# Kernel optimization log

Hardware: AMD Instinct MI355X
Metric: run time of the kernel (lower is better)

The kernel has to match this reference:

```python
import math
import jax, jax.numpy as jnp
import numpy as np
from jax import lax

B, T, D, S, N_SLOTS, N_ITERS = 16, 4096, 768, 768, 16, 8
THR, EPS = 0.5, 1e-8
SCALE = D ** -0.5
NEG = -jnp.finfo(jnp.float32).max


def ln(x, g, b):
    mu = x.mean(-1, keepdims=True)
    var = ((x - mu) ** 2).mean(-1, keepdims=True)
    return (x - mu) / jnp.sqrt(var + 1e-5) * g + b


def gru_cell(u, h, wih, whh, bih, bhh):
    # torch GRUCell: r,z,n gate ordering
    gi = u @ wih.T + bih
    gh = h @ whh.T + bhh
    ir, iz, inn = jnp.split(gi, 3, axis=-1)
    hr, hz, hn = jnp.split(gh, 3, axis=-1)
    r = jax.nn.sigmoid(ir + hr)
    z = jax.nn.sigmoid(iz + hz)
    n = jnp.tanh(inn + r * hn)
    return (1.0 - z) * n + z * h


def sa_step(slots, k, v, p, slot_mask, context_mask):
    q = ln(slots, p['lsg'], p['lsb']) @ p['Wq'].T
    dots = jnp.einsum('bid,bjd->bij', q, k) * SCALE  # [B, n_slots, T]
    dots = jnp.where(context_mask[:, None, :], dots, NEG)
    if slot_mask is not None:
        dots = jnp.where(slot_mask[:, :, None], dots, NEG)
    attn_vis = jax.nn.softmax(dots, axis=1)  # softmax over SLOTS (inverted attn)
    attn = attn_vis + EPS
    attn = attn / attn.sum(-1, keepdims=True)
    updates = jnp.einsum('bjd,bij->bid', v, attn)
    b, n, d = slots.shape
    h = gru_cell(updates.reshape(b * n, d), slots.reshape(b * n, d),
                 p['gwih'], p['gwhh'], p['gbih'], p['gbhh'])
    slots = h.reshape(b, n, d)
    pre = ln(slots, p['lfg'], p['lfb'])
    slots = slots + (jax.nn.relu(pre @ p['w1'].T + p['b1']) @ p['w2'].T + p['b2'])
    return slots, attn_vis


def cluster_single(slots, attn, slot_mask):
    sl = lax.stop_gradient(slots)  # torch no_grad block
    ns = sl / jnp.clip(jnp.linalg.norm(sl, axis=-1, keepdims=True), 1e-12)
    smm = (slot_mask[:, :, None] & slot_mask[:, None, :]).astype(jnp.float32)
    dist = 1.0 - jnp.einsum('bnd,bmd->bnm', ns, ns)
    dist = jnp.where(smm > 0, dist, 2.0)
    adj = (dist < THR).astype(jnp.float32) * smm
    for _ in range(math.ceil(math.log2(N_SLOTS))):  # transitive closure by squaring
        adj = jnp.minimum(adj @ adj, 1.0) * smm
    cum = jnp.cumsum(adj, axis=1)
    cm = adj * (cum <= 1.0)  # keep first row of each connected component
    counts = (cm > 0).any(axis=2).sum(axis=1)
    reset = counts < 3
    eye = jnp.eye(N_SLOTS, dtype=jnp.float32)[None] * slot_mask[:, :, None].astype(jnp.float32)
    cm = jnp.where(reset[:, None, None], eye, cm)
    cw = cm / jnp.clip(cm.sum(axis=2, keepdims=True), 1.0)
    cm = lax.stop_gradient(cm)
    cw = lax.stop_gradient(cw)
    means = cw @ slots          # grads flow through slots only
    cattn = cm @ attn           # grads flow through attn only
    out_mask = (cm > 0).any(axis=2) & slot_mask
    return means, cattn, out_mask


def setup_inputs() -> dict:
    key = jax.random.key(0)
    ks = jax.random.split(key, 16)
    sc = 0.02
    return {
        'x': jax.random.normal(ks[0], (B, T, D), jnp.float32),
        'context_mask': jnp.ones((B, T), jnp.bool_),
        'n_slots': N_SLOTS,
        'slots_init': jax.random.normal(ks[1], (N_SLOTS, S), jnp.float32),
        'Wk': jax.random.normal(ks[2], (S, D), jnp.float32) * sc,
        'Wv': jax.random.normal(ks[3], (S, D), jnp.float32) * sc,
        'Wq': jax.random.normal(ks[4], (S, S), jnp.float32) * sc,
        'gwih': jax.random.normal(ks[5], (3 * S, S), jnp.float32) * sc,
        'gwhh': jax.random.normal(ks[6], (3 * S, S), jnp.float32) * sc,
        'gbih': jnp.zeros((3 * S,), jnp.float32),
        'gbhh': jnp.zeros((3 * S,), jnp.float32),
        'w1': jax.random.normal(ks[7], (4 * S, S), jnp.float32) * sc,
        'b1': jnp.zeros((4 * S,), jnp.float32),
        'w2': jax.random.normal(ks[8], (S, 4 * S), jnp.float32) * sc,
        'b2': jnp.zeros((S,), jnp.float32),
        'lin_g': jnp.ones((D,), jnp.float32), 'lin_b': jnp.zeros((D,), jnp.float32),
        'lsg': jnp.ones((S,), jnp.float32), 'lsb': jnp.zeros((S,), jnp.float32),
        'lfg': jnp.ones((S,), jnp.float32), 'lfb': jnp.zeros((S,), jnp.float32),
    }


def reference(x, context_mask, n_slots, slots_init, Wk, Wv, Wq, gwih, gwhh,
              gbih, gbhh, w1, b1, w2, b2, lin_g, lin_b, lsg, lsb, lfg, lfb):
    p = dict(Wq=Wq, gwih=gwih, gwhh=gwhh, gbih=gbih, gbhh=gbhh,
             w1=w1, b1=b1, w2=w2, b2=b2, lsg=lsg, lsb=lsb, lfg=lfg, lfb=lfb)
    xn = ln(x, lin_g, lin_b)
    init_slots = jnp.broadcast_to(slots_init[None], (x.shape[0], N_SLOTS, S))
    k = xn @ Wk.T
    v = xn @ Wv.T
    slots = init_slots
    for _ in range(N_ITERS):
        slots, attn = sa_step(slots, k, v, p, None, context_mask)
    # implicit differentiation trick
    slots = lax.stop_gradient(slots) - lax.stop_gradient(init_slots) + init_slots
    slot_mask = jnp.ones((x.shape[0], N_SLOTS), jnp.bool_)
    slots, attn = sa_step(slots, k, v, p, slot_mask, context_mask)
    slots, attn, slot_mask = cluster_single(slots, attn, slot_mask)
    attn_map = jnp.transpose(attn, (0, 2, 1))  # [B, T, n_slots]
    return slots, attn_map, slot_mask
```

## Files before the change

### kernel.cpp

```cpp
#include <hip/hip_runtime.h>
#include <hip/hip_bf16.h>

typedef __hip_bfloat16 bf16;
typedef __attribute__((ext_vector_type(4))) float f32x4;
typedef __attribute__((ext_vector_type(8))) short s16x8;
typedef unsigned int u32;
typedef unsigned short u16;

#define B_ 16
#define T_ 4096
#define D_ 768
#define S_ 768
#define NS 16
#define NIT 9
#define NCHUNK 16
#define TCH 256
#define EPS 1e-8f
#define SCALE 0.036084391824351615f

__device__ __forceinline__ void gld16(const void* g, void* l) {
    __builtin_amdgcn_global_load_lds((const __attribute__((address_space(1))) u32*)g,
                                     (__attribute__((address_space(3))) u32*)l, 16, 0, 0);
}

__device__ __forceinline__ u16 bfbits(float x) {
    bf16 h = __float2bfloat16(x);
    return *reinterpret_cast<u16*>(&h);
}

__global__ void __launch_bounds__(256) cvt_all_kernel(
    const float* __restrict__ wq, const float* __restrict__ wk, const float* __restrict__ wv,
    const float* __restrict__ gwih, const float* __restrict__ gwhh,
    const float* __restrict__ w1, const float* __restrict__ w2,
    bf16* __restrict__ wq_b, bf16* __restrict__ wkv_b,
    bf16* __restrict__ gwih_b, bf16* __restrict__ gwhh_b,
    bf16* __restrict__ w1_b, bf16* __restrict__ w2_b)
{
    int i = blockIdx.x * 256 + threadIdx.x;
    const int NW = 589824, NG = 1769472, NM = 2359296;
    if (i < NW) { wq_b[i] = __float2bfloat16(wq[i]); return; }
    i -= NW;
    if (i < NW) { wkv_b[i] = __float2bfloat16(wk[i]); return; }
    i -= NW;
    if (i < NW) { wkv_b[NW + i] = __float2bfloat16(wv[i]); return; }
    i -= NW;
    if (i < NG) { gwih_b[i] = __float2bfloat16(gwih[i]); return; }
    i -= NG;
    if (i < NG) { gwhh_b[i] = __float2bfloat16(gwhh[i]); return; }
    i -= NG;
    if (i < NM) { w1_b[i] = __float2bfloat16(w1[i]); return; }
    i -= NM;
    w2_b[i] = __float2bfloat16(w2[i]);
}

__global__ void __launch_bounds__(256) ln768_kernel(
    const float* __restrict__ x, const float* __restrict__ g,
    const float* __restrict__ bta, bf16* __restrict__ out)
{
    int wid = threadIdx.x >> 6, lane = threadIdx.x & 63;
    int row = blockIdx.x * 4 + wid;
    const float4* xr = (const float4*)(x + (size_t)row * 768);
    float4 v[3];
    float s = 0.f;
    #pragma unroll
    for (int i = 0; i < 3; ++i) {
        v[i] = xr[lane + i * 64];
        s += v[i].x + v[i].y + v[i].z + v[i].w;
    }
    #pragma unroll
    for (int off = 1; off < 64; off <<= 1) s += __shfl_xor(s, off);
    float mu = s * (1.f / 768.f);
    float q = 0.f;
    #pragma unroll
    for (int i = 0; i < 3; ++i) {
        float a = v[i].x - mu, b = v[i].y - mu, c = v[i].z - mu, d = v[i].w - mu;
        q += a * a + b * b + c * c + d * d;
    }
    #pragma unroll
    for (int off = 1; off < 64; off <<= 1) q += __shfl_xor(q, off);
    float rs = rsqrtf(q * (1.f / 768.f) + 1e-5f);
    ushort4* orow = (ushort4*)(out + (size_t)row * 768);
    const float4* gg = (const float4*)g;
    const float4* bb = (const float4*)bta;
    #pragma unroll
    for (int i = 0; i < 3; ++i) {
        float4 gv = gg[lane + i * 64], bv = bb[lane + i * 64];
        ushort4 o;
        o.x = bfbits((v[i].x - mu) * rs * gv.x + bv.x);
        o.y = bfbits((v[i].y - mu) * rs * gv.y + bv.y);
        o.z = bfbits((v[i].z - mu) * rs * gv.z + bv.z);
        o.w = bfbits((v[i].w - mu) * rs * gv.w + bv.w);
        orow[lane + i * 64] = o;
    }
}

__global__ void __launch_bounds__(512) gemm256_kernel(
    const bf16* __restrict__ A, const bf16* __restrict__ W,
    bf16* __restrict__ kout, bf16* __restrict__ vTout, float* __restrict__ vsum)
{
    __shared__ char smem[49152];
    __shared__ float vs_l[128];
    bf16* As = (bf16*)smem;
    bf16* Bs = (bf16*)(smem + 32768);
    int tid = threadIdx.x, lane = tid & 63, wid = tid >> 6;
    int bid = blockIdx.x;
    int xcd = bid & 7, idx = bid >> 3;
    int mt = xcd * 32 + idx / 12;
    int nt = idx % 12;
    int bm0 = mt * 256, bn0 = nt * 128;
    int wr = wid >> 1, wc = wid & 1;
    int g = lane >> 4, r15 = lane & 15;
    const f32x4 vzero = {0.f, 0.f, 0.f, 0.f};
    f32x4 acc[4][4];
    #pragma unroll
    for (int m = 0; m < 4; ++m)
        #pragma unroll
        for (int n = 0; n < 4; ++n) acc[m][n] = vzero;

    for (int kt = 0; kt < 768; kt += 64) {
        __syncthreads();
        #pragma unroll
        for (int i = 0; i < 4; ++i) {
            int s0 = i * 512 + wid * 64;
            int o = (s0 + lane) * 16;
            int r = o >> 7, cb = o & 127;
            int cbs = cb ^ ((r & 7) << 4);
            gld16(A + (size_t)(bm0 + r) * 768 + kt + (cbs >> 1), (char*)As + (size_t)s0 * 16);
        }
        #pragma unroll
        for (int i = 0; i < 2; ++i) {
            int s0 = i * 512 + wid * 64;
            int o = (s0 + lane) * 16;
            int r = o >> 7, cb = o & 127;
            int cbs = cb ^ ((r & 7) << 4);
            gld16(W + (size_t)(bn0 + r) * 768 + kt + (cbs >> 1), (char*)Bs + (size_t)s0 * 16);
        }
        asm volatile("s_waitcnt vmcnt(0)" ::: "memory");
        __syncthreads();
        #pragma unroll
        for (int kk2 = 0; kk2 < 2; ++kk2) {
            s16x8 af[4], bfr[4];
            #pragma unroll
            for (int m = 0; m < 4; ++m) {
                int r = wr * 64 + m * 16 + r15;
                int p = r * 128 + ((kk2 * 64 + g * 16) ^ ((r & 7) << 4));
                af[m] = *(const s16x8*)((const char*)As + p);
            }
            #pragma unroll
            for (int n = 0; n < 4; ++n) {
                int r = wc * 64 + n * 16 + r15;
                int p = r * 128 + ((kk2 * 64 + g * 16) ^ ((r & 7) << 4));
                bfr[n] = *(const s16x8*)((const char*)Bs + p);
            }
            #pragma unroll
            for (int m = 0; m < 4; ++m)
                #pragma unroll
                for (int n = 0; n < 4; ++n)
                    acc[m][n] = __builtin_amdgcn_mfma_f32_16x16x32_bf16(af[m], bfr[n], acc[m][n], 0, 0, 0);
        }
    }

    bool is_v = (bn0 >= 768);
    float* Ct = (float*)smem;
    int bq = bm0 >> 12;
    int tloc = bm0 & 4095;
    if (is_v && tid < 128) vs_l[tid] = 0.f;
    #pragma unroll
    for (int q = 0; q < 4; ++q) {
        __syncthreads();
        if (wr == q) {
            #pragma unroll
            for (int m = 0; m < 4; ++m)
                #pragma unroll
                for (int n = 0; n < 4; ++n)
                    #pragma unroll
                    for (int j = 0; j < 4; ++j)
                        Ct[(m * 16 + g * 4 + j) * 132 + wc * 64 + n * 16 + r15] = acc[m][n][j];
        }
        __syncthreads();
        if (!is_v) {
            int r = tid >> 3, cq = tid & 7;
            u16 tmp[16];
            #pragma unroll
            for (int i = 0; i < 4; ++i) {
                f32x4 vv = *(const f32x4*)&Ct[r * 132 + cq * 16 + i * 4];
                #pragma unroll
                for (int jj = 0; jj < 4; ++jj) tmp[i * 4 + jj] = bfbits(vv[jj]);
            }
            s16x8 o0, o1;
            #pragma unroll
            for (int i = 0; i < 8; ++i) { o0[i] = (short)tmp[i]; o1[i] = (short)tmp[8 + i]; }
            bf16* dst = kout + (size_t)(bm0 + q * 64 + r) * 768 + bn0 + cq * 16;
            *(s16x8*)dst = o0;
            *(s16x8*)(dst + 8) = o1;
        } else {
            int d = tid >> 2, tq = tid & 3;
            float ssum = 0.f;
            u16 tmp[16];
            #pragma unroll
            for (int i = 0; i < 16; ++i) {
                float f = Ct[(tq * 16 + i) * 132 + d];
                ssum += f;
                tmp[i] = bfbits(f);
            }
            s16x8 o0, o1;
            #pragma unroll
            for (int i = 0; i < 8; ++i) { o0[i] = (short)tmp[i]; o1[i] = (short)tmp[8 + i]; }
            bf16* dst = vTout + ((size_t)bq * 768 + (bn0 - 768) + d) * (size_t)T_
                        + tloc + q * 64 + tq * 16;
            *(s16x8*)dst = o0;
            *(s16x8*)(dst + 8) = o1;
            atomicAdd(&vs_l[d], ssum);
        }
    }
    if (is_v) {
        __syncthreads();
        if (tid < 128) atomicAdd(vsum + bq * 768 + (bn0 - 768) + tid, vs_l[tid]);
    }
}

__global__ void init_slots_kernel(const float* __restrict__ si,
                                  float* __restrict__ slots, bf16* __restrict__ slots_bf)
{
    int idx = blockIdx.x * 256 + threadIdx.x;
    float v = si[idx % (NS * S_)];
    slots[idx] = v;
    slots_bf[idx] = __float2bfloat16(v);
}

__global__ void __launch_bounds__(256) ln_gemm_kernel(
    const float* __restrict__ xin, const float* __restrict__ gam, const float* __restrict__ bet,
    const bf16* __restrict__ W, const float* __restrict__ bias,
    bf16* __restrict__ out, int N, int relu)
{
    __shared__ bf16 As[16 * 768];
    __shared__ bf16 Ws[2][64 * 64];
    int tid = threadIdx.x;
    int bx = blockIdx.x, bn0 = blockIdx.y * 64;
    int row = tid >> 4, li = tid & 15;
    const float* xr = xin + (size_t)(bx * 16 + row) * 768;
    float vals[48];
    float s = 0.f;
    #pragma unroll
    for (int i = 0; i < 48; ++i) { vals[i] = xr[li + i * 16]; s += vals[i]; }
    #pragma unroll
    for (int m = 1; m < 16; m <<= 1) s += __shfl_xor(s, m);
    float mu = s * (1.f / 768.f);
    float q = 0.f;
    #pragma unroll
    for (int i = 0; i < 48; ++i) { float d = vals[i] - mu; q += d * d; }
    #pragma unroll
    for (int m = 1; m < 16; m <<= 1) q += __shfl_xor(q, m);
    float rs = rsqrtf(q * (1.f / 768.f) + 1e-5f);
    #pragma unroll
    for (int i = 0; i < 48; ++i) {
        int c = li + i * 16;
        float v = (vals[i] - mu) * rs * gam[c] + bet[c];
        *(u16*)((char*)As + row * 1536 + ((c * 2) ^ ((row & 7) << 4))) = bfbits(v);
    }
    int lane = tid & 63, wid = tid >> 6;
    int g = lane >> 4, s15 = lane & 15;
    auto stageW = [&](int kt, int buf) {
        #pragma unroll
        for (int i = 0; i < 2; ++i) {
            int s0 = i * 256 + wid * 64;
            int o = (s0 + lane) * 16;
            int r = o >> 7, cb = o & 127;
            int cbs = cb ^ ((r & 7) << 4);
            gld16(W + (size_t)(bn0 + r) * 768 + kt + (cbs >> 1),
                  (char*)Ws[buf] + (size_t)s0 * 16);
        }
    };
    stageW(0, 0);
    asm volatile("s_waitcnt vmcnt(0)" ::: "memory");
    __syncthreads();
    f32x4 acc = {0.f, 0.f, 0.f, 0.f};
    int rb = wid * 16 + s15;
    for (int t = 0; t < 12; ++t) {
        int cur = t & 1;
        if (t < 11) stageW((t + 1) * 64, cur ^ 1);
        #pragma unroll
        for (int kk2 = 0; kk2 < 2; ++kk2) {
            int kabs = t * 64 + kk2 * 32;
            s16x8 af = *(const s16x8*)((const char*)As + s15 * 1536 +
                                       ((kabs * 2 + g * 16) ^ ((s15 & 7) << 4)));
            s16x8 bf_ = *(const s16x8*)((const char*)Ws[cur] + rb * 128 +
                                        ((kk2 * 64 + g * 16) ^ ((rb & 7) << 4)));
            acc = __builtin_amdgcn_mfma_f32_16x16x32_bf16(af, bf_, acc, 0, 0, 0);
        }
        asm volatile("s_waitcnt vmcnt(0)" ::: "memory");
        __syncthreads();
    }
    int cn = bn0 + rb;
    float bv = bias ? bias[cn] : 0.f;
    #pragma unroll
    for (int j = 0; j < 4; ++j) {
        float val = acc[j] + bv;
        if (relu) val = fmaxf(val, 0.f);
        out[(size_t)(bx * 16 + g * 4 + j) * N + cn] = __float2bfloat16(val);
    }
}

__global__ void __launch_bounds__(256) gru_fused16_kernel(
    const bf16* __restrict__ upd, const bf16* __restrict__ slotsA_bf,
    const bf16* __restrict__ Wih, const bf16* __restrict__ Whh,
    const float* __restrict__ bih, const float* __restrict__ bhh,
    const float* __restrict__ slotsA, float* __restrict__ slotsB)
{
    __shared__ char sm[53248];
    int tid = threadIdx.x, lane = tid & 63, wid = tid >> 6;
    int g = lane >> 4, r15 = lane & 15;
    int bm0 = blockIdx.x * 16, bn0 = blockIdx.y * 64;
    const f32x4 vz = {0.f, 0.f, 0.f, 0.f};
    f32x4 acc[6] = {vz, vz, vz, vz, vz, vz};

    for (int kt = 0; kt < 768; kt += 64) {
        __syncthreads();
        #pragma unroll
        for (int i = 0; i < 13; ++i) {
            int s0 = i * 256 + wid * 64;
            int seg = s0 + lane;
            const bf16* src;
            if (seg < 256) {
                int ls = seg & 127;
                int o = ls * 16;
                int r = o >> 7, cb = o & 127;
                int cbs = cb ^ ((r & 7) << 4);
                const bf16* base = (seg < 128) ? upd : slotsA_bf;
                src = base + (size_t)(bm0 + r) * 768 + kt + (cbs >> 1);
            } else {
                int ws = seg - 256;
                int p = ws >> 9, qq = ws & 511;
                int o = qq * 16;
                int r = o >> 7, cb = o & 127;
                int cbs = cb ^ ((r & 7) << 4);
                src = (p < 3)
                    ? Wih + (size_t)(p * 768 + bn0 + r) * 768 + kt + (cbs >> 1)
                    : Whh + (size_t)((p - 3) * 768 + bn0 + r) * 768 + kt + (cbs >> 1);
            }
            gld16(src, sm + (size_t)s0 * 16);
        }
        asm volatile("s_waitcnt vmcnt(0)" ::: "memory");
        __syncthreads();
        #pragma unroll
        for (int kk2 = 0; kk2 < 2; ++kk2) {
            int pa = r15 * 128 + ((kk2 * 64 + g * 16) ^ ((r15 & 7) << 4));
            s16x8 au = *(const s16x8*)(sm + pa);
            s16x8 ah = *(const s16x8*)(sm + 2048 + pa);
            int rb = wid * 16 + r15;
            int pb = rb * 128 + ((kk2 * 64 + g * 16) ^ ((rb & 7) << 4));
            #pragma unroll
            for (int p = 0; p < 6; ++p) {
                s16x8 wf = *(const s16x8*)(sm + 4096 + p * 8192 + pb);
                acc[p] = __builtin_amdgcn_mfma_f32_16x16x32_bf16(
                    (p < 3) ? au : ah, wf, acc[p], 0, 0, 0);
            }
        }
    }
    int cn = bn0 + wid * 16 + r15;
    float bir = bih[cn], biz = bih[768 + cn], bin_ = bih[1536 + cn];
    float bhr = bhh[cn], bhz = bhh[768 + cn], bhn = bhh[1536 + cn];
    #pragma unroll
    for (int j = 0; j < 4; ++j) {
        int m = bm0 + g * 4 + j;
        float ir = acc[0][j] + bir, iz = acc[1][j] + biz, inn = acc[2][j] + bin_;
        float hr = acc[3][j] + bhr, hz = acc[4][j] + bhz, hn = acc[5][j] + bhn;
        float rg = 1.f / (1.f + expf(-(ir + hr)));
        float z  = 1.f / (1.f + expf(-(iz + hz)));
        float nn = tanhf(inn + rg * hn);
        float h  = slotsA[(size_t)m * 768 + cn];
        slotsB[(size_t)m * 768 + cn] = (1.f - z) * nn + z * h;
    }
}

__device__ __forceinline__ void skinny_body(
    const bf16* A, const bf16* Bm, const float* bias, const float* Cin,
    float* Cf, bf16* Cb, int N, int K, int bm0, int bn0, int relu,
    bf16* As, bf16* Bs)
{
    int tid = threadIdx.x, lane = tid & 63, wid = tid >> 6;
    int g = lane >> 4, r15 = lane & 15;
    f32x4 acc = {0.f, 0.f, 0.f, 0.f};
    for (int kt = 0; kt < K; kt += 64) {
        __syncthreads();
        #pragma unroll
        for (int i = 0; i < 3; ++i) {
            int s0 = i * 256 + wid * 64;
            if (s0 < 640) {
                int o = (s0 + lane) * 16;
                if (o < 2048) {
                    int r = o >> 7, cb = o & 127;
                    int cbs = cb ^ ((r & 7) << 4);
                    gld16(A + (size_t)(bm0 + r) * K + kt + (cbs >> 1), (char*)As + (size_t)s0 * 16);
                } else {
                    int ob = o - 2048;
                    int r = ob >> 7, cb = ob & 127;
                    int cbs = cb ^ ((r & 7) << 4);
                    gld16(Bm + (size_t)(bn0 + r) * K + kt + (cbs >> 1),
                          (char*)Bs + (size_t)(s0 * 16 - 2048));
                }
            }
        }
        asm volatile("s_waitcnt vmcnt(0)" ::: "memory");
        __syncthreads();
        #pragma unroll
        for (int kk = 0; kk < 64; kk += 32) {
            int pa = r15 * 128 + ((kk * 2 + g * 16) ^ ((r15 & 7) << 4));
            s16x8 af = *(const s16x8*)((const char*)As + pa);
            int rb = wid * 16 + r15;
            int pb = rb * 128 + ((kk * 2 + g * 16) ^ ((rb & 7) << 4));
            s16x8 bfr = *(const s16x8*)((const char*)Bs + pb);
            acc = __builtin_amdgcn_mfma_f32_16x16x32_bf16(af, bfr, acc, 0, 0, 0);
        }
    }
    int cn = bn0 + wid * 16 + r15;
    float bv = bias ? bias[cn] : 0.f;
    #pragma unroll
    for (int j = 0; j < 4; ++j) {
        int cm = bm0 + g * 4 + j;
        size_t ci = (size_t)cm * N + cn;
        float val = acc[j] + bv;
        if (Cin) val += Cin[ci];
        if (relu) val = fmaxf(val, 0.f);
        if (Cf) Cf[ci] = val;
        if (Cb) Cb[ci] = __float2bfloat16(val);
    }
}

__global__ void __launch_bounds__(256) mlp2_kernel(
    const bf16* __restrict__ h1, const bf16* __restrict__ W2, const float* __restrict__ b2,
    const float* __restrict__ slotsB, float* __restrict__ slotsA, bf16* __restrict__ slotsA_bf)
{
    __shared__ bf16 As[16 * 64];
    __shared__ bf16 Bs[64 * 64];
    skinny_body(h1, W2, b2, slotsB, slotsA, slotsA_bf, 768, 3072,
                blockIdx.x * 16, blockIdx.y * 64, 0, As, Bs);
}

__global__ void __launch_bounds__(256) fused_attn_kernel(
    const bf16* __restrict__ q_bf, const bf16* __restrict__ k_bf, const bf16* __restrict__ vT,
    float* __restrict__ pU, float* __restrict__ prs, float* __restrict__ avis, int write_avis)
{
    __shared__ char smem[131072];
    bf16* ks0 = (bf16*)smem;
    bf16* ks1 = (bf16*)(smem + 49152);
    bf16* qs  = (bf16*)(smem + 98304);
    char* aL  = smem + 122880;
    __shared__ float rsw[2][16];
    int tid = threadIdx.x, lane = tid & 63, wid = tid >> 6;
    int b = blockIdx.x >> 4, chunk = blockIdx.x & 15;
    int t0 = chunk * TCH;
    int g = lane >> 4, s15 = lane & 15;
    const bf16* qb  = q_bf + (size_t)b * 16 * 768;
    const bf16* kb  = k_bf + (size_t)b * T_ * 768;
    const bf16* vtb = vT + (size_t)b * 768 * (size_t)T_;

    auto stage_k = [&](int tb, bf16* dst) {
        #pragma unroll
        for (int i = 0; i < 12; ++i) {
            int s0 = i * 256 + wid * 64;
            int o = (s0 + lane) * 16;
            int r = o / 1536, cb = o % 1536;
            int cbs = cb ^ ((r & 7) << 4);
            gld16(kb + (size_t)(tb + r) * 768 + (cbs >> 1), (char*)dst + (size_t)s0 * 16);
        }
    };
    auto stage_v = [&](int tb, bf16* dst) {
        #pragma unroll
        for (int i = 0; i < 12; ++i) {
            int s0 = i * 256 + wid * 64;
            int o = (s0 + lane) * 16;
            int d = o >> 6, cb = o & 63;
            int cbs = cb ^ ((d & 3) << 4);
            gld16(vtb + (size_t)d * T_ + tb + (cbs >> 1), (char*)dst + (size_t)s0 * 16);
        }
    };

    #pragma unroll
    for (int i = 0; i < 6; ++i) {
        int s0 = i * 256 + wid * 64;
        int o = (s0 + lane) * 16;
        int r = o / 1536, cb = o % 1536;
        int cbs = cb ^ ((r & 7) << 4);
        gld16(qb + (size_t)r * 768 + (cbs >> 1), (char*)qs + (size_t)s0 * 16);
    }
    stage_k(t0, ks0);
    asm volatile("s_waitcnt vmcnt(0)" ::: "memory");
    __syncthreads();

    const f32x4 vzero = {0.f, 0.f, 0.f, 0.f};
    float rs_acc = 0.f;

    for (int ts = 0; ts < 8; ++ts) {
        bf16* cur = (ts & 1) ? ks1 : ks0;
        bf16* nxt = (ts & 1) ? ks0 : ks1;
        if (ts < 7) stage_k(t0 + (ts + 1) * 32, nxt);
        if (wid < 2) {
            f32x4 dacc = vzero;
            #pragma unroll
            for (int kk = 0; kk < 768; kk += 32) {
                int rk = wid * 16 + s15;
                int pk = rk * 1536 + ((kk * 2 + g * 16) ^ ((rk & 7) << 4));
                s16x8 kf = *(const s16x8*)((const char*)cur + pk);
                int pq = s15 * 1536 + ((kk * 2 + g * 16) ^ ((s15 & 7) << 4));
                s16x8 qf = *(const s16x8*)((const char*)qs + pq);
                dacc = __builtin_amdgcn_mfma_f32_16x16x32_bf16(kf, qf, dacc, 0, 0, 0);
            }
            float d0 = dacc[0] * SCALE, d1 = dacc[1] * SCALE,
                  d2 = dacc[2] * SCALE, d3 = dacc[3] * SCALE;
            float m0 = d0, m1 = d1, m2 = d2, m3 = d3;
            #pragma unroll
            for (int off = 1; off < 16; off <<= 1) {
                m0 = fmaxf(m0, __shfl_xor(m0, off));
                m1 = fmaxf(m1, __shfl_xor(m1, off));
                m2 = fmaxf(m2, __shfl_xor(m2, off));
                m3 = fmaxf(m3, __shfl_xor(m3, off));
            }
            float e0 = expf(d0 - m0), e1 = expf(d1 - m1), e2 = expf(d2 - m2), e3 = expf(d3 - m3);
            float q0 = e0, q1 = e1, q2 = e2, q3 = e3;
            #pragma unroll
            for (int off = 1; off < 16; off <<= 1) {
                q0 += __shfl_xor(q0, off);
                q1 += __shfl_xor(q1, off);
                q2 += __shfl_xor(q2, off);
                q3 += __shfl_xor(q3, off);
            }
            float a0 = e0 / q0, a1 = e1 / q1, a2 = e2 / q2, a3 = e3 / q3;
            rs_acc += a0 + a1 + a2 + a3;
            int tl = wid * 16 + g * 4;
            ushort2 p0, p1;
            p0.x = bfbits(a0); p0.y = bfbits(a1);
            p1.x = bfbits(a2); p1.y = bfbits(a3);
            int sw = (s15 & 3) << 4;
            char* aS = aL + ts * 1024;
            *(ushort2*)(aS + s15 * 64 + ((tl * 2) ^ sw))       = p0;
            *(ushort2*)(aS + s15 * 64 + (((tl + 2) * 2) ^ sw)) = p1;
            if (write_avis) {
                f32x4 wv = {a0, a1, a2, a3};
                *(f32x4*)(avis + (size_t)(b * 16 + s15) * T_ + t0 + ts * 32 + tl) = wv;
            }
        }
        asm volatile("s_waitcnt vmcnt(0)" ::: "memory");
        __syncthreads();
    }

    f32x4 uacc[12];
    #pragma unroll
    for (int i = 0; i < 12; ++i) uacc[i] = vzero;
    stage_v(t0, ks0);
    asm volatile("s_waitcnt vmcnt(0)" ::: "memory");
    __syncthreads();
    for (int ts = 0; ts < 8; ++ts) {
        bf16* cur = (ts & 1) ? ks1 : ks0;
        bf16* nxt = (ts & 1) ? ks0 : ks1;
        if (ts < 7) stage_v(t0 + (ts + 1) * 32, nxt);
        {
            int pa = ts * 1024 + s15 * 64 + ((g * 16) ^ ((s15 & 3) << 4));
            s16x8 afr = *(const s16x8*)(aL + pa);
            #pragma unroll
            for (int i = 0; i < 12; ++i) {
                int d = (wid * 12 + i) * 16 + s15;
                int pv = d * 64 + ((g * 16) ^ ((d & 3) << 4));
                s16x8 vf = *(const s16x8*)((const char*)cur + pv);
                uacc[i] = __builtin_amdgcn_mfma_f32_16x16x32_bf16(vf, afr, uacc[i], 0, 0, 0);
            }
        }
        asm volatile("s_waitcnt vmcnt(0)" ::: "memory");
        __syncthreads();
    }

    float* pUb = pU + (size_t)(b * 16 + chunk) * 768 * 16;
    #pragma unroll
    for (int i = 0; i < 12; ++i) {
        int dbase = (wid * 12 + i) * 16 + g * 4;
        #pragma unroll
        for (int j = 0; j < 4; ++j)
            pUb[(size_t)(dbase + j) * 16 + s15] = uacc[i][j];
    }
    rs_acc += __shfl_xor(rs_acc, 16);
    rs_acc += __shfl_xor(rs_acc, 32);
    if (wid < 2 && lane < 16) rsw[wid][s15] = rs_acc;
    __syncthreads();
    if (tid < 16) prs[(b * 16 + chunk) * 16 + tid] = rsw[0][tid] + rsw[1][tid];
}

__global__ void __launch_bounds__(256) attn_reduce_kernel(
    const float* __restrict__ pU, const float* __restrict__ prs,
    const float* __restrict__ vsum, bf16* __restrict__ upd)
{
    int idx = blockIdx.x * 256 + threadIdx.x;
    int d = idx % 768;
    int s = (idx / 768) & 15;
    int b = idx / (768 * 16);
    float su = 0.f;
    #pragma unroll
    for (int c = 0; c < 16; ++c) su += pU[((size_t)(b * 16 + c) * 768 + d) * 16 + s];
    float rs = 0.f;
    #pragma unroll
    for (int c = 0; c < 16; ++c) rs += prs[(b * 16 + c) * 16 + s];
    float val = (su + EPS * vsum[b * 768 + d]) / (rs + T_ * EPS);
    upd[idx] = __float2bfloat16(val);
}

__global__ void __launch_bounds__(256) cluster_kernel(
    const float* __restrict__ slots, float* __restrict__ out_slots,
    float* __restrict__ out_mask, float* __restrict__ cm_g)
{
    int b = blockIdx.x;
    __shared__ float s[16][768];
    __shared__ float inv[16];
    __shared__ float adj[16][16], tmp[16][16], cw[16][16];
    __shared__ int reset_s;
    const float* sb = slots + (size_t)b * 16 * 768;
    for (int i = threadIdx.x; i < 16 * 768; i += 256) s[i / 768][i % 768] = sb[i];
    __syncthreads();
    if (threadIdx.x < 16) {
        float q = 0.f;
        for (int d = 0; d < 768; ++d) q += s[threadIdx.x][d] * s[threadIdx.x][d];
        inv[threadIdx.x] = 1.f / fmaxf(sqrtf(q), 1e-12f);
    }
    __syncthreads();
    int n = threadIdx.x >> 4, m = threadIdx.x & 15;
    float dot = 0.f;
    for (int d = 0; d < 768; ++d) dot += s[n][d] * s[m][d];
    dot *= inv[n] * inv[m];
    adj[n][m] = ((1.f - dot) < 0.5f) ? 1.f : 0.f;
    __syncthreads();
    #pragma unroll
    for (int it = 0; it < 4; ++it) {
        float t = 0.f;
        #pragma unroll
        for (int j = 0; j < 16; ++j) t += adj[n][j] * adj[j][m];
        tmp[n][m] = fminf(t, 1.f);
        __syncthreads();
        adj[n][m] = tmp[n][m];
        __syncthreads();
    }
    if (threadIdx.x < 16) {
        int mm = threadIdx.x;
        float run = 0.f;
        for (int nn = 0; nn < 16; ++nn) {
            run += adj[nn][mm];
            tmp[nn][mm] = adj[nn][mm] * ((run <= 1.f) ? 1.f : 0.f);
        }
    }
    __syncthreads();
    if (threadIdx.x == 0) {
        int cnt2 = 0;
        for (int nn = 0; nn < 16; ++nn) {
            bool any = false;
            for (int j = 0; j < 16; ++j) any = any || (tmp[nn][j] > 0.f);
            cnt2 += any ? 1 : 0;
        }
        reset_s = (cnt2 < 3) ? 1 : 0;
    }
    __syncthreads();
    if (reset_s) tmp[n][m] = (n == m) ? 1.f : 0.f;
    __syncthreads();
    if (threadIdx.x < 16) {
        float rs = 0.f;
        for (int j = 0; j < 16; ++j) rs += tmp[threadIdx.x][j];
        rs = fmaxf(rs, 1.f);
        for (int j = 0; j < 16; ++j) cw[threadIdx.x][j] = tmp[threadIdx.x][j] / rs;
        bool any = false;
        for (int j = 0; j < 16; ++j) any = any || (tmp[threadIdx.x][j] > 0.f);
        out_mask[b * 16 + threadIdx.x] = any ? 1.f : 0.f;
    }
    cm_g[b * 256 + threadIdx.x] = tmp[n][m];
    __syncthreads();
    for (int i = threadIdx.x; i < 16 * 768; i += 256) {
        int nn = i / 768, d = i - nn * 768;
        float acc = 0.f;
        #pragma unroll
        for (int j = 0; j < 16; ++j) acc += cw[nn][j] * s[j][d];
        out_slots[(size_t)b * 16 * 768 + i] = acc;
    }
}

__global__ void __launch_bounds__(256) cattn_kernel(
    const float* __restrict__ av, const float* __restrict__ cm_g, float* __restrict__ out_attn)
{
    int b = blockIdx.y;
    int t = blockIdx.x * 256 + threadIdx.x;
    __shared__ float cm[16][16];
    cm[threadIdx.x >> 4][threadIdx.x & 15] = cm_g[b * 256 + threadIdx.x];
    __syncthreads();
    float avv[16];
    #pragma unroll
    for (int j = 0; j < 16; ++j) avv[j] = av[((size_t)b * 16 + j) * T_ + t];
    #pragma unroll
    for (int i = 0; i < 16; ++i) {
        float acc = 0.f;
        #pragma unroll
        for (int j = 0; j < 16; ++j) acc += cm[i][j] * avv[j];
        out_attn[((size_t)b * T_ + t) * 16 + i] = acc;
    }
}

extern "C" void kernel_launch(void* const* d_in, const int* in_sizes, int n_in,
                              void* d_out, int out_size, void* d_ws, size_t ws_size,
                              hipStream_t stream)
{
    const float* x    = (const float*)d_in[0];
    const float* si   = (const float*)d_in[3];
    const float* Wk   = (const float*)d_in[4];
    const float* Wv   = (const float*)d_in[5];
    const float* Wq   = (const float*)d_in[6];
    const float* gwih = (const float*)d_in[7];
    const float* gwhh = (const float*)d_in[8];
    const float* gbih = (const float*)d_in[9];
    const float* gbhh = (const float*)d_in[10];
    const float* w1   = (const float*)d_in[11];
    const float* b1   = (const float*)d_in[12];
    const float* w2   = (const float*)d_in[13];
    const float* b2   = (const float*)d_in[14];
    const float* ling = (const float*)d_in[15];
    const float* linb = (const float*)d_in[16];
    const float* lsg  = (const float*)d_in[17];
    const float* lsb  = (const float*)d_in[18];
    const float* lfg  = (const float*)d_in[19];
    const float* lfb  = (const float*)d_in[20];

    char* w = (char*)d_ws;
    size_t off = 0;
    auto alloc = [&](size_t bytes) { void* p = w + off; off += (bytes + 255) & ~(size_t)255; return p; };
    bf16* xn     = (bf16*)alloc((size_t)B_ * T_ * D_ * 2);
    bf16* k_bf   = (bf16*)alloc((size_t)B_ * T_ * S_ * 2);
    bf16* vT     = (bf16*)alloc((size_t)B_ * S_ * T_ * 2);
    float* avis  = (float*)alloc((size_t)B_ * NS * T_ * 4);
    float* pU    = (float*)alloc((size_t)B_ * NCHUNK * S_ * NS * 4);
    float* prs   = (float*)alloc((size_t)B_ * NCHUNK * NS * 4);
    float* vsum  = (float*)alloc((size_t)B_ * S_ * 4);
    float* slotsA = (float*)alloc((size_t)B_ * NS * S_ * 4);
    bf16* slotsA_bf = (bf16*)alloc((size_t)B_ * NS * S_ * 2);
    float* slotsB = (float*)alloc((size_t)B_ * NS * S_ * 4);
    bf16* q_bf   = (bf16*)alloc((size_t)B_ * NS * S_ * 2);
    bf16* upd_bf = (bf16*)alloc((size_t)B_ * NS * S_ * 2);
    bf16* h1_bf  = (bf16*)alloc((size_t)B_ * NS * 4 * S_ * 2);
    bf16* wq_bf  = (bf16*)alloc((size_t)S_ * S_ * 2);
    bf16* wkv_bf = (bf16*)alloc((size_t)1536 * D_ * 2);
    bf16* gwih_bf = (bf16*)alloc((size_t)3 * S_ * S_ * 2);
    bf16* gwhh_bf = (bf16*)alloc((size_t)3 * S_ * S_ * 2);
    bf16* w1_bf  = (bf16*)alloc((size_t)4 * S_ * S_ * 2);
    bf16* w2_bf  = (bf16*)alloc((size_t)S_ * 4 * S_ * 2);
    float* cm_g  = (float*)alloc((size_t)B_ * 256 * 4);

    float* out_slots = (float*)d_out;
    float* out_attn  = out_slots + (size_t)B_ * NS * S_;
    float* out_mask  = out_attn + (size_t)B_ * T_ * NS;

    cvt_all_kernel<<<39168, 256, 0, stream>>>(Wq, Wk, Wv, gwih, gwhh, w1, w2,
                                              wq_bf, wkv_bf, gwih_bf, gwhh_bf, w1_bf, w2_bf);

    ln768_kernel<<<B_ * T_ / 4, 256, 0, stream>>>(x, ling, linb, xn);

    (void)hipMemsetAsync(vsum, 0, (size_t)B_ * S_ * 4, stream);
    gemm256_kernel<<<3072, 512, 0, stream>>>(xn, wkv_bf, k_bf, vT, vsum);

    init_slots_kernel<<<(B_ * NS * S_) / 256, 256, 0, stream>>>(si, slotsA, slotsA_bf);

    for (int it = 0; it < NIT; ++it) {
        {
            dim3 g(16, 12);
            ln_gemm_kernel<<<g, 256, 0, stream>>>(slotsA, lsg, lsb, wq_bf, nullptr,
                                                  q_bf, 768, 0);
        }
        fused_attn_kernel<<<B_ * NCHUNK, 256, 0, stream>>>(q_bf, k_bf, vT, pU, prs, avis,
                                                           (it == NIT - 1) ? 1 : 0);
        attn_reduce_kernel<<<(B_ * NS * S_) / 256, 256, 0, stream>>>(pU, prs, vsum, upd_bf);
        {
            dim3 g(16, 12);
            gru_fused16_kernel<<<g, 256, 0, stream>>>(upd_bf, slotsA_bf, gwih_bf, gwhh_bf,
                                                      gbih, gbhh, slotsA, slotsB);
        }
        {
            dim3 g(16, 48);
            ln_gemm_kernel<<<g, 256, 0, stream>>>(slotsB, lfg, lfb, w1_bf, b1,
                                                  h1_bf, 3072, 1);
        }
        {
            dim3 g(16, 12);
            mlp2_kernel<<<g, 256, 0, stream>>>(h1_bf, w2_bf, b2, slotsB, slotsA, slotsA_bf);
        }
    }

    cluster_kernel<<<B_, 256, 0, stream>>>(slotsA, out_slots, out_mask, cm_g);
    {
        dim3 g(T_ / 256, B_);
        cattn_kernel<<<g, 256, 0, stream>>>(avis, cm_g, out_attn);
    }
}
```

Measured before the change: 1.478 ms.

## Shrink attention LDS footprint by half-width staging and register-resident queries

Shared memory in the fused attention kernel drops from 128KB to 56KB. K and V tiles are now staged in half-width pieces (384 columns or rows) through a double buffer, and q fragments are held in registers instead of LDS. The aim is to fit more blocks per CU and overlap the loads better. In exchange it uses many more VGPRs for the 24 q fragments and adds extra barriers per tile, which may limit occupancy anyway.

```diff
diff --git a/kernel.cpp b/kernel.cpp
--- a/kernel.cpp
+++ b/kernel.cpp
@@ -441,11 +441,10 @@
     const bf16* __restrict__ q_bf, const bf16* __restrict__ k_bf, const bf16* __restrict__ vT,
     float* __restrict__ pU, float* __restrict__ prs, float* __restrict__ avis, int write_avis)
 {
-    __shared__ char smem[131072];
+    __shared__ char smem[57344];
     bf16* ks0 = (bf16*)smem;
-    bf16* ks1 = (bf16*)(smem + 49152);
-    bf16* qs  = (bf16*)(smem + 98304);
-    char* aL  = smem + 122880;
+    bf16* ks1 = (bf16*)(smem + 24576);
+    char* aL  = smem + 49152;
     __shared__ float rsw[2][16];
     int tid = threadIdx.x, lane = tid & 63, wid = tid >> 6;
     int b = blockIdx.x >> 4, chunk = blockIdx.x & 15;
@@ -455,128 +454,168 @@
     const bf16* kb  = k_bf + (size_t)b * T_ * 768;
     const bf16* vtb = vT + (size_t)b * 768 * (size_t)T_;
 
-    auto stage_k = [&](int tb, bf16* dst) {
-        #pragma unroll
-        for (int i = 0; i < 12; ++i) {
+    auto stage_kh = [&](int tb, int kh, bf16* dst) {
+        #pragma unroll
+        for (int i = 0; i < 6; ++i) {
             int s0 = i * 256 + wid * 64;
             int o = (s0 + lane) * 16;
-            int r = o / 1536, cb = o % 1536;
+            int r = o / 768, cb = o % 768;
             int cbs = cb ^ ((r & 7) << 4);
-            gld16(kb + (size_t)(tb + r) * 768 + (cbs >> 1), (char*)dst + (size_t)s0 * 16);
+            gld16(kb + (size_t)(tb + r) * 768 + kh * 384 + (cbs >> 1),
+                  (char*)dst + (size_t)s0 * 16);
         }
     };
-    auto stage_v = [&](int tb, bf16* dst) {
-        #pragma unroll
-        for (int i = 0; i < 12; ++i) {
+    auto stage_vh = [&](int tb, int dh, bf16* dst) {
+        #pragma unroll
+        for (int i = 0; i < 6; ++i) {
             int s0 = i * 256 + wid * 64;
             int o = (s0 + lane) * 16;
             int d = o >> 6, cb = o & 63;
             int cbs = cb ^ ((d & 3) << 4);
-            gld16(vtb + (size_t)d * T_ + tb + (cbs >> 1), (char*)dst + (size_t)s0 * 16);
+            gld16(vtb + (size_t)(dh * 384 + d) * T_ + tb + (cbs >> 1),
+                  (char*)dst + (size_t)s0 * 16);
         }
     };
 
-    #pragma unroll
-    for (int i = 0; i < 6; ++i) {
-        int s0 = i * 256 + wid * 64;
-        int o = (s0 + lane) * 16;
-        int r = o / 1536, cb = o % 1536;
-        int cbs = cb ^ ((r & 7) << 4);
-        gld16(qb + (size_t)r * 768 + (cbs >> 1), (char*)qs + (size_t)s0 * 16);
-    }
-    stage_k(t0, ks0);
-    asm volatile("s_waitcnt vmcnt(0)" ::: "memory");
-    __syncthreads();
+    s16x8 qreg[24];
+    #pragma unroll
+    for (int i = 0; i < 24; ++i)
+        qreg[i] = *(const s16x8*)(qb + (size_t)s15 * 768 + i * 32 + g * 8);
 
     const f32x4 vzero = {0.f, 0.f, 0.f, 0.f};
     float rs_acc = 0.f;
 
-    for (int ts = 0; ts < 8; ++ts) {
-        bf16* cur = (ts & 1) ? ks1 : ks0;
-        bf16* nxt = (ts & 1) ? ks0 : ks1;
-        if (ts < 7) stage_k(t0 + (ts + 1) * 32, nxt);
-        if (wid < 2) {
-            f32x4 dacc = vzero;
-            #pragma unroll
-            for (int kk = 0; kk < 768; kk += 32) {
-                int rk = wid * 16 + s15;
-                int pk = rk * 1536 + ((kk * 2 + g * 16) ^ ((rk & 7) << 4));
-                s16x8 kf = *(const s16x8*)((const char*)cur + pk);
-                int pq = s15 * 1536 + ((kk * 2 + g * 16) ^ ((s15 & 7) << 4));
-                s16x8 qf = *(const s16x8*)((const char*)qs + pq);
-                dacc = __builtin_amdgcn_mfma_f32_16x16x32_bf16(kf, qf, dacc, 0, 0, 0);
-            }
-            float d0 = dacc[0] * SCALE, d1 = dacc[1] * SCALE,
-                  d2 = dacc[2] * SCALE, d3 = dacc[3] * SCALE;
-            float m0 = d0, m1 = d1, m2 = d2, m3 = d3;
-            #pragma unroll
-            for (int off = 1; off < 16; off <<= 1) {
-                m0 = fmaxf(m0, __shfl_xor(m0, off));
-                m1 = fmaxf(m1, __shfl_xor(m1, off));
-                m2 = fmaxf(m2, __shfl_xor(m2, off));
-                m3 = fmaxf(m3, __shfl_xor(m3, off));
-            }
-            float e0 = expf(d0 - m0), e1 = expf(d1 - m1), e2 = expf(d2 - m2), e3 = expf(d3 - m3);
-            float q0 = e0, q1 = e1, q2 = e2, q3 = e3;
-            #pragma unroll
-            for (int off = 1; off < 16; off <<= 1) {
-                q0 += __shfl_xor(q0, off);
-                q1 += __shfl_xor(q1, off);
-                q2 += __shfl_xor(q2, off);
-                q3 += __shfl_xor(q3, off);
-            }
-            float a0 = e0 / q0, a1 = e1 / q1, a2 = e2 / q2, a3 = e3 / q3;
-            rs_acc += a0 + a1 + a2 + a3;
-            int tl = wid * 16 + g * 4;
-            ushort2 p0, p1;
-            p0.x = bfbits(a0); p0.y = bfbits(a1);
-            p1.x = bfbits(a2); p1.y = bfbits(a3);
-            int sw = (s15 & 3) << 4;
-            char* aS = aL + ts * 1024;
-            *(ushort2*)(aS + s15 * 64 + ((tl * 2) ^ sw))       = p0;
-            *(ushort2*)(aS + s15 * 64 + (((tl + 2) * 2) ^ sw)) = p1;
-            if (write_avis) {
-                f32x4 wv = {a0, a1, a2, a3};
-                *(f32x4*)(avis + (size_t)(b * 16 + s15) * T_ + t0 + ts * 32 + tl) = wv;
-            }
-        }
-        asm volatile("s_waitcnt vmcnt(0)" ::: "memory");
-        __syncthreads();
+    {
+        bf16* cur = ks0;
+        bf16* nxt = ks1;
+        stage_kh(t0, 0, cur);
+        f32x4 dacc = vzero;
+        for (int ts = 0; ts < 8; ++ts) {
+            int tb = t0 + ts * 32;
+            stage_kh(tb, 1, nxt);
+            asm volatile("s_waitcnt vmcnt(6)" ::: "memory");
+            __syncthreads();
+            if (wid < 2) {
+                dacc = vzero;
+                #pragma unroll
+                for (int ii = 0; ii < 12; ++ii) {
+                    int rk = wid * 16 + s15;
+                    int pk = rk * 768 + ((ii * 64 + g * 16) ^ ((rk & 7) << 4));
+                    s16x8 kf = *(const s16x8*)((const char*)cur + pk);
+                    dacc = __builtin_amdgcn_mfma_f32_16x16x32_bf16(kf, qreg[ii], dacc, 0, 0, 0);
+                }
+            }
+            __syncthreads();
+            { bf16* t = cur; cur = nxt; nxt = t; }
+            if (ts < 7) {
+                stage_kh(tb + 32, 0, nxt);
+                asm volatile("s_waitcnt vmcnt(6)" ::: "memory");
+            } else {
+                asm volatile("s_waitcnt vmcnt(0)" ::: "memory");
+            }
+            __syncthreads();
+            if (wid < 2) {
+                #pragma unroll
+                for (int ii = 0; ii < 12; ++ii) {
+                    int rk = wid * 16 + s15;
+                    int pk = rk * 768 + ((ii * 64 + g * 16) ^ ((rk & 7) << 4));
+                    s16x8 kf = *(const s16x8*)((const char*)cur + pk);
+                    dacc = __builtin_amdgcn_mfma_f32_16x16x32_bf16(kf, qreg[12 + ii], dacc, 0, 0, 0);
+                }
+                float d0 = dacc[0] * SCALE, d1 = dacc[1] * SCALE,
+                      d2 = dacc[2] * SCALE, d3 = dacc[3] * SCALE;
+                float m0 = d0, m1 = d1, m2 = d2, m3 = d3;
+                #pragma unroll
+                for (int off = 1; off < 16; off <<= 1) {
+                    m0 = fmaxf(m0, __shfl_xor(m0, off));
+                    m1 = fmaxf(m1, __shfl_xor(m1, off));
+                    m2 = fmaxf(m2, __shfl_xor(m2, off));
+                    m3 = fmaxf(m3, __shfl_xor(m3, off));
+                }
+                float e0 = expf(d0 - m0), e1 = expf(d1 - m1), e2 = expf(d2 - m2), e3 = expf(d3 - m3);
+                float q0 = e0, q1 = e1, q2 = e2, q3 = e3;
+                #pragma unroll
+                for (int off = 1; off < 16; off <<= 1) {
+                    q0 += __shfl_xor(q0, off);
+                    q1 += __shfl_xor(q1, off);
+                    q2 += __shfl_xor(q2, off);
+                    q3 += __shfl_xor(q3, off);
+                }
+                float a0 = e0 / q0, a1 = e1 / q1, a2 = e2 / q2, a3 = e3 / q3;
+                rs_acc += a0 + a1 + a2 + a3;
+                int tl = wid * 16 + g * 4;
+                ushort2 p0, p1;
+                p0.x = bfbits(a0); p0.y = bfbits(a1);
+                p1.x = bfbits(a2); p1.y = bfbits(a3);
+                int sw = (s15 & 3) << 4;
+                char* aS = aL + ts * 1024;
+                *(ushort2*)(aS + s15 * 64 + ((tl * 2) ^ sw))       = p0;
+                *(ushort2*)(aS + s15 * 64 + (((tl + 2) * 2) ^ sw)) = p1;
+                if (write_avis) {
+                    f32x4 wv = {a0, a1, a2, a3};
+                    *(f32x4*)(avis + (size_t)(b * 16 + s15) * T_ + tb + tl) = wv;
+                }
+            }
+            __syncthreads();
+            { bf16* t = cur; cur = nxt; nxt = t; }
+        }
     }
 
     f32x4 uacc[12];
     #pragma unroll
     for (int i = 0; i < 12; ++i) uacc[i] = vzero;
-    stage_v(t0, ks0);
-    asm volatile("s_waitcnt vmcnt(0)" ::: "memory");
-    __syncthreads();
-    for (int ts = 0; ts < 8; ++ts) {
-        bf16* cur = (ts & 1) ? ks1 : ks0;
-        bf16* nxt = (ts & 1) ? ks0 : ks1;
-        if (ts < 7) stage_v(t0 + (ts + 1) * 32, nxt);
-        {
-            int pa = ts * 1024 + s15 * 64 + ((g * 16) ^ ((s15 & 3) << 4));
-            s16x8 afr = *(const s16x8*)(aL + pa);
-            #pragma unroll
-            for (int i = 0; i < 12; ++i) {
-                int d = (wid * 12 + i) * 16 + s15;
-                int pv = d * 64 + ((g * 16) ^ ((d & 3) << 4));
+    {
+        bf16* cur = ks0;
+        bf16* nxt = ks1;
+        stage_vh(t0, 0, cur);
+        for (int ts = 0; ts < 8; ++ts) {
+            int tb = t0 + ts * 32;
+            s16x8 afr;
+            {
+                int pa = ts * 1024 + s15 * 64 + ((g * 16) ^ ((s15 & 3) << 4));
+                afr = *(const s16x8*)(aL + pa);
+            }
+            stage_vh(tb, 1, nxt);
+            asm volatile("s_waitcnt vmcnt(6)" ::: "memory");
+            __syncthreads();
+            #pragma unroll
+            for (int i = 0; i < 6; ++i) {
+                int dl = (wid * 6 + i) * 16 + s15;
+                int pv = dl * 64 + ((g * 16) ^ ((dl & 3) << 4));
                 s16x8 vf = *(const s16x8*)((const char*)cur + pv);
                 uacc[i] = __builtin_amdgcn_mfma_f32_16x16x32_bf16(vf, afr, uacc[i], 0, 0, 0);
             }
-        }
-        asm volatile("s_waitcnt vmcnt(0)" ::: "memory");
-        __syncthreads();
+            __syncthreads();
+            { bf16* t = cur; cur = nxt; nxt = t; }
+            if (ts < 7) {
+                stage_vh(tb + 32, 0, nxt);
+                asm volatile("s_waitcnt vmcnt(6)" ::: "memory");
+            } else {
+                asm volatile("s_waitcnt vmcnt(0)" ::: "memory");
+            }
+            __syncthreads();
+            #pragma unroll
+            for (int i = 0; i < 6; ++i) {
+                int dl = (wid * 6 + i) * 16 + s15;
+                int pv = dl * 64 + ((g * 16) ^ ((dl & 3) << 4));
+                s16x8 vf = *(const s16x8*)((const char*)cur + pv);
+                uacc[6 + i] = __builtin_amdgcn_mfma_f32_16x16x32_bf16(vf, afr, uacc[6 + i], 0, 0, 0);
+            }
+            __syncthreads();
+            { bf16* t = cur; cur = nxt; nxt = t; }
+        }
     }
 
     float* pUb = pU + (size_t)(b * 16 + chunk) * 768 * 16;
     #pragma unroll
-    for (int i = 0; i < 12; ++i) {
-        int dbase = (wid * 12 + i) * 16 + g * 4;
-        #pragma unroll
-        for (int j = 0; j < 4; ++j)
-            pUb[(size_t)(dbase + j) * 16 + s15] = uacc[i][j];
-    }
+    for (int dh = 0; dh < 2; ++dh)
+        #pragma unroll
+        for (int i = 0; i < 6; ++i) {
+            int dbase = dh * 384 + (wid * 6 + i) * 16 + g * 4;
+            #pragma unroll
+            for (int j = 0; j < 4; ++j)
+                pUb[(size_t)(dbase + j) * 16 + s15] = uacc[dh * 6 + i][j];
+        }
     rs_acc += __shfl_xor(rs_acc, 16);
     rs_acc += __shfl_xor(rs_acc, 32);
     if (wid < 2 && lane < 16) rsw[wid][s15] = rs_acc;
```

Result: slower. 1.534 ms (+3.8%).
